# Optimization experiments

Measured on AMD Instinct MI355X. Metric: run time of the kernel, lower is better.

## Reference

```python
import jax, jax.numpy as jnp
import numpy as np

SR = 32000
N_FFT = 1024
HOP = 320
N_MELS = 128
PCEN_S = 0.025
PCEN_ALPHA = 0.98
PCEN_DELTA = 2.0
PCEN_R = 0.5
EPS = 1e-06


def _mel_filterbank():
    # torchaudio melscale_fbanks defaults: HTK mel scale, norm=None, f_min=0, f_max=sr/2
    n_freqs = N_FFT // 2 + 1
    all_freqs = np.linspace(0.0, SR / 2.0, n_freqs)
    def hz_to_mel(f):
        return 2595.0 * np.log10(1.0 + f / 700.0)
    def mel_to_hz(m):
        return 700.0 * (10.0 ** (m / 2595.0) - 1.0)
    m_pts = np.linspace(hz_to_mel(0.0), hz_to_mel(SR / 2.0), N_MELS + 2)
    f_pts = mel_to_hz(m_pts)
    f_diff = f_pts[1:] - f_pts[:-1]                      # (n_mels+1,)
    slopes = f_pts[None, :] - all_freqs[:, None]          # (n_freqs, n_mels+2)
    down = -slopes[:, :-2] / f_diff[:-1]
    up = slopes[:, 2:] / f_diff[1:]
    fb = np.maximum(0.0, np.minimum(down, up))            # (n_freqs, n_mels)
    return jnp.asarray(fb, dtype=jnp.float32)


def _mel_spectrogram(x):
    # x: [B, 1, L]; torch.stft semantics: center=True, reflect pad, periodic hann, power=1
    pad = N_FFT // 2
    xp = jnp.pad(x, ((0, 0), (0, 0), (pad, pad)), mode='reflect')
    L = xp.shape[-1]
    n_frames = 1 + (L - N_FFT) // HOP                      # 401
    idx = jnp.arange(n_frames)[:, None] * HOP + jnp.arange(N_FFT)[None, :]
    frames = xp[..., idx]                                  # [B, 1, T, n_fft]
    n = jnp.arange(N_FFT, dtype=jnp.float32)
    window = 0.5 * (1.0 - jnp.cos(2.0 * jnp.pi * n / N_FFT))  # periodic hann
    spec = jnp.abs(jnp.fft.rfft(frames * window, axis=-1))    # [B, 1, T, F]
    fb = _mel_filterbank()                                    # [F, n_mels]
    mel = jnp.einsum('bctf,fm->bcmt', spec, fb)               # [B, 1, n_mels, T]
    return mel


def _pcen_iir(mel, s):
    # first-order recurrence M_t = (1-s) M_{t-1} + s x_t, M_0 = x_0, along last axis
    xt = jnp.moveaxis(mel, -1, 0)                          # [T, B, 1, M]
    def step(carry, x_t):
        m = (1.0 - s) * carry + s * x_t
        return m, m
    _, rest = jax.lax.scan(step, xt[0], xt[1:])
    M = jnp.concatenate([xt[:1], rest], axis=0)
    return jnp.moveaxis(M, 0, -1)


def setup_inputs() -> dict:
    key = jax.random.key(0)
    x = jax.random.normal(key, (128, 1, 128000), dtype=jnp.float32)
    return {"x": x}


def reference(x):
    mel = _mel_spectrogram(x)                              # [B,1,128,401]
    mel_smooth = _pcen_iir(mel, PCEN_S)
    smooth = jnp.power(EPS + mel_smooth, PCEN_ALPHA)
    pcen = jnp.power(mel / smooth + PCEN_DELTA, PCEN_R) - PCEN_DELTA ** PCEN_R
    mean = jnp.mean(pcen, axis=(2, 3), keepdims=True)
    std = jnp.std(pcen, axis=(2, 3), keepdims=True, ddof=1)  # torch std is unbiased
    return (pcen - mean) / (std + 1e-06)
```

## Files before the change

kernel.cpp:

```cpp
#include <hip/hip_runtime.h>
#include <math.h>

#define SR        32000
#define NFFT      1024
#define HOP       320
#define NMELS     128
#define NFREQS    513
#define LIN       128000
#define PADL      512
#define TFRAMES   401
#define NB        128

#define WS_WIN    0
#define WS_FB     1024
#define WS_FS     66688
#define WS_FE     66816
#define WS_T1     66944
#define WS_T2     68992
#define WS_PART   69120
#define WS_MEL    71168

__global__ void prep_kernel(float* __restrict__ win, float* __restrict__ fb,
                            int* __restrict__ fstart, int* __restrict__ fend,
                            float2* __restrict__ T1, float2* __restrict__ T2) {
    const int tid = threadIdx.x;

    for (int i = tid; i < NFFT; i += 256) {
        double ang = 2.0 * M_PI * (double)i / (double)NFFT;
        win[i] = (float)(0.5 - 0.5 * cos(ang));
    }

    for (int idx = tid; idx < 1024; idx += 256) {
        int tt = idx >> 4, k1 = idx & 15;
        double ang = -2.0 * M_PI * (double)(tt * k1) / 1024.0;
        T1[idx] = make_float2((float)cos(ang), (float)sin(ang));
    }
    if (tid < 64) {
        int s = tid >> 4, k2 = tid & 15;
        double ang = -2.0 * M_PI * (double)(s * k2) / 64.0;
        T2[tid] = make_float2((float)cos(ang), (float)sin(ang));
    }

    if (tid < NMELS) {
        const int m = tid;
        const double mel_max = 2595.0 * log10(1.0 + ((double)SR * 0.5) / 700.0);
        const double m0 = (double)(m)     * mel_max / (double)(NMELS + 1);
        const double m1 = (double)(m + 1) * mel_max / (double)(NMELS + 1);
        const double m2 = (double)(m + 2) * mel_max / (double)(NMELS + 1);
        const double f0 = 700.0 * (pow(10.0, m0 / 2595.0) - 1.0);
        const double f1 = 700.0 * (pow(10.0, m1 / 2595.0) - 1.0);
        const double f2 = 700.0 * (pow(10.0, m2 / 2595.0) - 1.0);
        const double binw = (double)SR * 0.5 / (double)(NFREQS - 1);
        int fs = (int)(f0 / binw) + 1;
        int fe = (int)ceil(f2 / binw);
        fs = (fs > 0) ? fs - 1 : 0;
        fe = (fe < NFREQS) ? fe + 1 : NFREQS;
        for (int f = fs; f < fe; ++f) {
            double freq = (double)f * binw;
            double down = (freq - f0) / (f1 - f0);
            double up   = (f2 - freq) / (f2 - f1);
            double v = fmin(down, up);
            v = fmax(0.0, v);
            fb[f * NMELS + m] = (float)v;
        }
        fstart[m] = fs;
        fend[m]   = fe;
    }
}

__device__ __forceinline__ void dft16(float (&xr)[16], float (&xi)[16]) {
    const float C8 = 0.92387953251128674f;
    const float S8 = 0.38268343236508978f;
    const float R2 = 0.70710678118654752f;
    const float WR[4][4] = {{1,1,1,1},{1, C8, R2, S8},{1, R2, 0.f,-R2},{1, S8,-R2,-C8}};
    const float WI[4][4] = {{0,0,0,0},{0,-S8,-R2,-C8},{0,-R2,-1.f,-R2},{0,-C8,-R2, S8}};
    float pr[4][4], pi[4][4];
#pragma unroll
    for (int j0 = 0; j0 < 4; ++j0) {
        float ar = xr[j0],      ai = xi[j0];
        float br = xr[j0 + 4],  bi = xi[j0 + 4];
        float cr = xr[j0 + 8],  ci = xi[j0 + 8];
        float dr = xr[j0 + 12], di = xi[j0 + 12];
        float t0r = ar + cr, t0i = ai + ci;
        float t1r = ar - cr, t1i = ai - ci;
        float t2r = br + dr, t2i = bi + di;
        float t3r = br - dr, t3i = bi - di;
        pr[j0][0] = t0r + t2r; pi[j0][0] = t0i + t2i;
        pr[j0][1] = t1r + t3i; pi[j0][1] = t1i - t3r;
        pr[j0][2] = t0r - t2r; pi[j0][2] = t0i - t2i;
        pr[j0][3] = t1r - t3i; pi[j0][3] = t1i + t3r;
    }
#pragma unroll
    for (int ka = 0; ka < 4; ++ka) {
        float q0r = pr[0][ka], q0i = pi[0][ka];
        float q1r = pr[1][ka] * WR[1][ka] - pi[1][ka] * WI[1][ka];
        float q1i = pr[1][ka] * WI[1][ka] + pi[1][ka] * WR[1][ka];
        float q2r = pr[2][ka] * WR[2][ka] - pi[2][ka] * WI[2][ka];
        float q2i = pr[2][ka] * WI[2][ka] + pi[2][ka] * WR[2][ka];
        float q3r = pr[3][ka] * WR[3][ka] - pi[3][ka] * WI[3][ka];
        float q3i = pr[3][ka] * WI[3][ka] + pi[3][ka] * WR[3][ka];
        float t0r = q0r + q2r, t0i = q0i + q2i;
        float t1r = q0r - q2r, t1i = q0i - q2i;
        float t2r = q1r + q3r, t2i = q1i + q3i;
        float t3r = q1r - q3r, t3i = q1i - q3i;
        xr[ka]      = t0r + t2r; xi[ka]      = t0i + t2i;
        xr[ka + 4]  = t1r + t3i; xi[ka + 4]  = t1i - t3r;
        xr[ka + 8]  = t0r - t2r; xi[ka + 8]  = t0i - t2i;
        xr[ka + 12] = t1r - t3i; xi[ka + 12] = t1i + t3r;
    }
}

__launch_bounds__(256)
__global__ void fft_mel_kernel(const float* __restrict__ x,
                               const float* __restrict__ win,
                               const float2* __restrict__ T1,
                               const float2* __restrict__ T2,
                               const float* __restrict__ fb,
                               const int* __restrict__ fstart,
                               const int* __restrict__ fend,
                               float* __restrict__ mel) {
    __shared__ __align__(16) float2 buf[4][NFFT];

    const int w = threadIdx.x >> 6;
    const int t = threadIdx.x & 63;
    const int bid  = (blockIdx.x & 7) * 802 + (blockIdx.x >> 3);
    const int task = bid * 4 + w;
    const int q  = task / TFRAMES;
    const int tf = task - q * TFRAMES;
    const float* xb0 = x + (size_t)(2 * q) * LIN;
    const float* xb1 = xb0 + LIN;
    const int base = tf * HOP - PADL;

    float4 t1v[8];
    {
        const float4* T1v = (const float4*)T1;
#pragma unroll
        for (int r = 0; r < 8; ++r) t1v[r] = T1v[t * 8 + r];
    }

    float xr[16], xi[16];
    if (base >= 0 && base + NFFT <= LIN) {
#pragma unroll
        for (int j = 0; j < 16; ++j) {
            int n = t + 64 * j;
            float wv = win[n];
            xr[j] = xb0[base + n] * wv;
            xi[j] = xb1[base + n] * wv;
        }
    } else {
#pragma unroll
        for (int j = 0; j < 16; ++j) {
            int n = t + 64 * j;
            int p = base + n;
            p = (p < 0) ? -p : p;
            p = (p >= LIN) ? (2 * LIN - 2 - p) : p;
            float wv = win[n];
            xr[j] = xb0[p] * wv;
            xi[j] = xb1[p] * wv;
        }
    }

    dft16(xr, xi);
#pragma unroll
    for (int k1 = 1; k1 < 16; ++k1) {
        const int r = k1 >> 1;
        const float2 wv = (k1 & 1) ? make_float2(t1v[r].z, t1v[r].w)
                                   : make_float2(t1v[r].x, t1v[r].y);
        const float tr = xr[k1] * wv.x - xi[k1] * wv.y;
        xi[k1] = xr[k1] * wv.y + xi[k1] * wv.x;
        xr[k1] = tr;
    }

    float2* B = buf[w];
#pragma unroll
    for (int k1 = 0; k1 < 16; ++k1)
        B[k1 * 64 + (t ^ ((k1 & 3) << 2))] = make_float2(xr[k1], xi[k1]);

    const int g = t >> 2, s = t & 3;
    const int c2 = g & 3;
#pragma unroll
    for (int j = 0; j < 16; ++j) {
        float2 v = B[g * 64 + s + 4 * (j ^ c2)];
        xr[j] = v.x; xi[j] = v.y;
    }

    dft16(xr, xi);
    {
        const float2* __restrict__ Tr = T2 + (s << 4);
#pragma unroll
        for (int k2 = 1; k2 < 16; ++k2) {
            const float2 wv = Tr[k2];
            const float tr = xr[k2] * wv.x - xi[k2] * wv.y;
            xi[k2] = xr[k2] * wv.y + xi[k2] * wv.x;
            xr[k2] = tr;
        }
    }

    {
        const int g2 = (g & 7) << 1;
#pragma unroll
        for (int k2 = 0; k2 < 16; ++k2)
            B[g * 64 + ((4 * k2 + s) ^ g2)] = make_float2(xr[k2], xi[k2]);
    }

    const float4* Bv = (const float4*)buf[w];
    const int gk = t & 15;
    const int g2k = (gk & 7) << 1;
    const int tb = t >> 4;
    float m0r[8], m1r[8];
#pragma unroll
    for (int jj = 0; jj < 8; ++jj) {
        const int k  = t + 64 * jj;
        const int jk = (tb + 4 * jj) & 15;
        const int e0 = gk * 64 + ((4 * jk) ^ g2k);
        float4 E01 = Bv[e0 >> 1];
        float4 E23 = Bv[(e0 ^ 2) >> 1];
        float S02r = E01.x + E23.x, S02i = E01.y + E23.y;
        float D02r = E01.x - E23.x, D02i = E01.y - E23.y;
        float S13r = E01.z + E23.z, S13i = E01.w + E23.w;
        float D13r = E01.z - E23.z, D13i = E01.w - E23.w;
        float a, b;
        if (jj < 4) { a = S02r + S13r; b = S02i + S13i; }
        else        { a = D02r + D13i; b = D02i - D13r; }
        const int kN = (1024 - k) & 1023;
        const int gN = kN & 15, jN = (kN >> 4) & 15, bN = kN >> 8;
        const int eN = gN * 64 + ((4 * jN) ^ ((gN & 7) << 1));
        float4 F01 = Bv[eN >> 1];
        float4 F23 = Bv[(eN ^ 2) >> 1];
        float GS02r = F01.x + F23.x, GS02i = F01.y + F23.y;
        float GD02r = F01.x - F23.x, GD02i = F01.y - F23.y;
        float GS13r = F01.z + F23.z, GS13i = F01.w + F23.w;
        float GD13r = F01.z - F23.z, GD13i = F01.w - F23.w;
        const float sE = (bN & 2) ? -1.0f : 1.0f;
        float cEv = GS02r + sE * GS13r, dEv = GS02i + sE * GS13i;
        float cOv = GD02r + sE * GD13i, dOv = GD02i - sE * GD13r;
        float c = (bN & 1) ? cOv : cEv;
        float d = (bN & 1) ? dOv : dEv;
        m0r[jj] = 0.5f * sqrtf((a + c) * (a + c) + (b - d) * (b - d));
        m1r[jj] = 0.5f * sqrtf((b + d) * (b + d) + (c - a) * (c - a));
    }
    float e512a = 0.0f, e512b = 0.0f;
    if (t == 0) {
        float4 E01 = Bv[0], E23 = Bv[1];
        e512a = fabsf((E01.x + E23.x) - (E01.z + E23.z));
        e512b = fabsf((E01.y + E23.y) - (E01.w + E23.w));
    }

    float2* mag2 = buf[w];
#pragma unroll
    for (int jj = 0; jj < 8; ++jj)
        mag2[t + 64 * jj] = make_float2(m0r[jj], m1r[jj]);
    if (t == 0) mag2[512] = make_float2(e512a, e512b);

#pragma unroll
    for (int h = 0; h < 2; ++h) {
        const int m = t + 64 * h;
        const int fs = fstart[m], fe = fend[m];
        const float* fr = fb + m;
        float a0 = 0.0f, a1 = 0.0f;
        for (int f = fs; f < fe; ++f) {
            float2 mg = mag2[f];
            float cf = fr[f * NMELS];
            a0 = fmaf(mg.x, cf, a0);
            a1 = fmaf(mg.y, cf, a1);
        }
        mel[((size_t)(2 * q)     * TFRAMES + tf) * NMELS + m] = a0;
        mel[((size_t)(2 * q + 1) * TFRAMES + tf) * NMELS + m] = a1;
    }
}

#define CHUNKS 8
#define CH0LEN 51
#define CHLEN  50
#define AFACT  0.2819890f

__launch_bounds__(256)
__global__ void pcen_kernel(const float* __restrict__ mel,
                            float* __restrict__ out,
                            double* __restrict__ partials) {
    const int b   = blockIdx.x >> 2;
    const int mg  = blockIdx.x & 3;
    const int tid = threadIdx.x;
    const int ml  = tid & 31;
    const int c   = tid >> 5;
    const int m   = mg * 32 + ml;
    const int t0  = (c == 0) ? 0 : (CH0LEN + CHLEN * (c - 1));
    const int len = (c == 0) ? CH0LEN : CHLEN;
    const float* mb = mel + (size_t)b * TFRAMES * NMELS;

    float v[CH0LEN];
#pragma unroll
    for (int i = 0; i < CH0LEN; ++i)
        if (i < len) v[i] = mb[(size_t)(t0 + i) * NMELS + m];

    float M;
    if (c == 0) {
        M = v[0];
#pragma unroll
        for (int i = 1; i < CH0LEN; ++i) M = fmaf(0.975f, M, 0.025f * v[i]);
    } else {
        M = 0.0f;
#pragma unroll
        for (int i = 0; i < CHLEN; ++i) M = fmaf(0.975f, M, 0.025f * v[i]);
    }
    __shared__ float Bc[CHUNKS][32];
    Bc[c][ml] = M;
    __syncthreads();

    float Min = 0.0f;
    if (c > 0) {
        Min = Bc[0][ml];
        for (int k = 1; k < c; ++k) Min = fmaf(AFACT, Min, Bc[k][ml]);
    }

    M = Min;
    float sum = 0.0f, sumsq = 0.0f;
    float* orow = out + (size_t)b * NMELS * TFRAMES + (size_t)m * TFRAMES + t0;
#pragma unroll
    for (int i = 0; i < CH0LEN; ++i) {
        if (i < len) {
            float xt = v[i];
            M = (c == 0 && i == 0) ? xt : fmaf(0.975f, M, 0.025f * xt);
            float rsm = __expf(-0.98f * __logf(1e-6f + M));
            float p = sqrtf(fmaf(xt, rsm, 2.0f)) - 1.4142135623730951f;
            orow[i] = p;
            sum += p;
            sumsq = fmaf(p, p, sumsq);
        }
    }

    double s = (double)sum, qq = (double)sumsq;
    for (int off = 32; off > 0; off >>= 1) {
        s  += __shfl_down(s, off);
        qq += __shfl_down(qq, off);
    }
    __shared__ double wsum[4], wsq[4];
    const int wid = tid >> 6, lane = tid & 63;
    if (lane == 0) { wsum[wid] = s; wsq[wid] = qq; }
    __syncthreads();
    if (tid == 0) {
        double S = wsum[0] + wsum[1] + wsum[2] + wsum[3];
        double Q = wsq[0] + wsq[1] + wsq[2] + wsq[3];
        partials[(size_t)(b * 4 + mg) * 2]     = S;
        partials[(size_t)(b * 4 + mg) * 2 + 1] = Q;
    }
}

__global__ void norm_kernel(float* __restrict__ out, const double* __restrict__ partials) {
    __shared__ float sh[2];
    const int b = blockIdx.x;
    if (threadIdx.x == 0) {
        double S = 0.0, Q = 0.0;
#pragma unroll
        for (int gg = 0; gg < 4; ++gg) {
            S += partials[(size_t)(b * 4 + gg) * 2];
            Q += partials[(size_t)(b * 4 + gg) * 2 + 1];
        }
        const double n = (double)(NMELS * TFRAMES);
        double mean = S / n;
        double var  = (Q - n * mean * mean) / (n - 1.0);
        double sd   = sqrt(var > 0.0 ? var : 0.0);
        sh[0] = (float)mean;
        sh[1] = (float)(1.0 / (sd + 1e-6));
    }
    __syncthreads();
    const int i4 = blockIdx.y * 256 + threadIdx.x;
    if (i4 >= NMELS * TFRAMES / 4) return;
    const float mean = sh[0], inv = sh[1];
    float4* o = (float4*)(out + (size_t)b * NMELS * TFRAMES);
    float4 vv = o[i4];
    vv.x = (vv.x - mean) * inv;
    vv.y = (vv.y - mean) * inv;
    vv.z = (vv.z - mean) * inv;
    vv.w = (vv.w - mean) * inv;
    o[i4] = vv;
}

extern "C" void kernel_launch(void* const* d_in, const int* in_sizes, int n_in,
                              void* d_out, int out_size, void* d_ws, size_t ws_size,
                              hipStream_t stream) {
    const float* x = (const float*)d_in[0];
    float* out = (float*)d_out;
    float* ws  = (float*)d_ws;

    float*  win    = ws + WS_WIN;
    float*  fb     = ws + WS_FB;
    int*    fstart = (int*)(ws + WS_FS);
    int*    fend   = (int*)(ws + WS_FE);
    float2* T1     = (float2*)(ws + WS_T1);
    float2* T2     = (float2*)(ws + WS_T2);
    double* parts  = (double*)(ws + WS_PART);
    float*  mel    = ws + WS_MEL;

    prep_kernel<<<dim3(1), dim3(256), 0, stream>>>(win, fb, fstart, fend, T1, T2);
    fft_mel_kernel<<<dim3((NB / 2) * TFRAMES / 4), dim3(256), 0, stream>>>(
        x, win, T1, T2, fb, fstart, fend, mel);
    pcen_kernel<<<dim3(NB * 4), dim3(256), 0, stream>>>(mel, out, parts);
    norm_kernel<<<dim3(NB, 51), dim3(256), 0, stream>>>(out, parts);
}
```

Baseline: 234.6 us.

## Pack mel filterbank into fixed-width band table and use one-wave FFT blocks

Replaces the dense 513x128 filterbank and variable-length per-mel loops with a packed 32-wide transposed band table, so the mel projection becomes a fully unrolled fixed loop with coalesced coefficient loads. The FFT/mel kernel moves from 256-thread blocks holding four frames to 64-thread single-wave blocks, and the prep kernel is spread across 9 blocks. The fixed width relies on every mel triangle spanning at most 32 bins, and the shorter bands now do redundant multiply-by-zero work.

```diff
diff --git a/kernel.cpp b/kernel.cpp
--- a/kernel.cpp
+++ b/kernel.cpp
@@ -10,37 +10,40 @@
 #define PADL      512
 #define TFRAMES   401
 #define NB        128
+#define FBW       32
 
 #define WS_WIN    0
-#define WS_FB     1024
-#define WS_FS     66688
-#define WS_FE     66816
-#define WS_T1     66944
-#define WS_T2     68992
-#define WS_PART   69120
-#define WS_MEL    71168
-
-__global__ void prep_kernel(float* __restrict__ win, float* __restrict__ fb,
-                            int* __restrict__ fstart, int* __restrict__ fend,
+#define WS_FBP    1024
+#define WS_FS     5120
+#define WS_T1     5248
+#define WS_T2     7296
+#define WS_PART   7424
+#define WS_MEL    9472
+
+__global__ void prep_kernel(float* __restrict__ win, float* __restrict__ fbpackT,
+                            int* __restrict__ fstart,
                             float2* __restrict__ T1, float2* __restrict__ T2) {
+    const int b   = blockIdx.x;
     const int tid = threadIdx.x;
 
-    for (int i = tid; i < NFFT; i += 256) {
+    if (b < 4) {
+        const int i = b * 256 + tid;
         double ang = 2.0 * M_PI * (double)i / (double)NFFT;
         win[i] = (float)(0.5 - 0.5 * cos(ang));
-    }
-
-    for (int idx = tid; idx < 1024; idx += 256) {
+        return;
+    }
+    if (b < 8) {
+        const int idx = (b - 4) * 256 + tid;
         int tt = idx >> 4, k1 = idx & 15;
         double ang = -2.0 * M_PI * (double)(tt * k1) / 1024.0;
         T1[idx] = make_float2((float)cos(ang), (float)sin(ang));
+        return;
     }
     if (tid < 64) {
         int s = tid >> 4, k2 = tid & 15;
         double ang = -2.0 * M_PI * (double)(s * k2) / 64.0;
         T2[tid] = make_float2((float)cos(ang), (float)sin(ang));
     }
-
     if (tid < NMELS) {
         const int m = tid;
         const double mel_max = 2595.0 * log10(1.0 + ((double)SR * 0.5) / 700.0);
@@ -51,20 +54,23 @@
         const double f1 = 700.0 * (pow(10.0, m1 / 2595.0) - 1.0);
         const double f2 = 700.0 * (pow(10.0, m2 / 2595.0) - 1.0);
         const double binw = (double)SR * 0.5 / (double)(NFREQS - 1);
-        int fs = (int)(f0 / binw) + 1;
-        int fe = (int)ceil(f2 / binw);
-        fs = (fs > 0) ? fs - 1 : 0;
-        fe = (fe < NFREQS) ? fe + 1 : NFREQS;
-        for (int f = fs; f < fe; ++f) {
-            double freq = (double)f * binw;
-            double down = (freq - f0) / (f1 - f0);
-            double up   = (f2 - freq) / (f2 - f1);
-            double v = fmin(down, up);
-            v = fmax(0.0, v);
-            fb[f * NMELS + m] = (float)v;
+        int fs = (int)(f0 / binw);
+        if (fs < 0) fs = 0;
+        int fe = (int)ceil(f2 / binw) + 1;
+        if (fe > NFREQS) fe = NFREQS;
+        for (int i = 0; i < FBW; ++i) {
+            const int f = fs + i;
+            float w = 0.0f;
+            if (f < fe) {
+                double freq = (double)f * binw;
+                double down = (freq - f0) / (f1 - f0);
+                double up   = (f2 - freq) / (f2 - f1);
+                double v = fmin(down, up);
+                w = (float)fmax(0.0, v);
+            }
+            fbpackT[i * NMELS + m] = w;
         }
         fstart[m] = fs;
-        fend[m]   = fe;
     }
 }
 
@@ -110,21 +116,18 @@
     }
 }
 
-__launch_bounds__(256)
+__launch_bounds__(64)
 __global__ void fft_mel_kernel(const float* __restrict__ x,
                                const float* __restrict__ win,
                                const float2* __restrict__ T1,
                                const float2* __restrict__ T2,
-                               const float* __restrict__ fb,
+                               const float* __restrict__ fbpackT,
                                const int* __restrict__ fstart,
-                               const int* __restrict__ fend,
                                float* __restrict__ mel) {
-    __shared__ __align__(16) float2 buf[4][NFFT];
-
-    const int w = threadIdx.x >> 6;
-    const int t = threadIdx.x & 63;
-    const int bid  = (blockIdx.x & 7) * 802 + (blockIdx.x >> 3);
-    const int task = bid * 4 + w;
+    __shared__ __align__(16) float2 buf[NFFT];
+
+    const int t = threadIdx.x;
+    const int task = (blockIdx.x & 7) * 3208 + (blockIdx.x >> 3);
     const int q  = task / TFRAMES;
     const int tf = task - q * TFRAMES;
     const float* xb0 = x + (size_t)(2 * q) * LIN;
@@ -171,7 +174,7 @@
         xr[k1] = tr;
     }
 
-    float2* B = buf[w];
+    float2* B = buf;
 #pragma unroll
     for (int k1 = 0; k1 < 16; ++k1)
         B[k1 * 64 + (t ^ ((k1 & 3) << 2))] = make_float2(xr[k1], xi[k1]);
@@ -203,7 +206,7 @@
             B[g * 64 + ((4 * k2 + s) ^ g2)] = make_float2(xr[k2], xi[k2]);
     }
 
-    const float4* Bv = (const float4*)buf[w];
+    const float4* Bv = (const float4*)buf;
     const int gk = t & 15;
     const int g2k = (gk & 7) << 1;
     const int tb = t >> 4;
@@ -246,7 +249,7 @@
         e512b = fabsf((E01.y + E23.y) - (E01.w + E23.w));
     }
 
-    float2* mag2 = buf[w];
+    float2* mag2 = buf;
 #pragma unroll
     for (int jj = 0; jj < 8; ++jj)
         mag2[t + 64 * jj] = make_float2(m0r[jj], m1r[jj]);
@@ -255,12 +258,14 @@
 #pragma unroll
     for (int h = 0; h < 2; ++h) {
         const int m = t + 64 * h;
-        const int fs = fstart[m], fe = fend[m];
-        const float* fr = fb + m;
+        const int fs = fstart[m];
         float a0 = 0.0f, a1 = 0.0f;
-        for (int f = fs; f < fe; ++f) {
-            float2 mg = mag2[f];
-            float cf = fr[f * NMELS];
+#pragma unroll
+        for (int i = 0; i < FBW; ++i) {
+            const float cf = fbpackT[i * NMELS + m];
+            int f = fs + i;
+            f = (f > 512) ? 512 : f;
+            const float2 mg = mag2[f];
             a0 = fmaf(mg.x, cf, a0);
             a1 = fmaf(mg.y, cf, a1);
         }
@@ -383,18 +388,17 @@
     float* out = (float*)d_out;
     float* ws  = (float*)d_ws;
 
-    float*  win    = ws + WS_WIN;
-    float*  fb     = ws + WS_FB;
-    int*    fstart = (int*)(ws + WS_FS);
-    int*    fend   = (int*)(ws + WS_FE);
-    float2* T1     = (float2*)(ws + WS_T1);
-    float2* T2     = (float2*)(ws + WS_T2);
-    double* parts  = (double*)(ws + WS_PART);
-    float*  mel    = ws + WS_MEL;
-
-    prep_kernel<<<dim3(1), dim3(256), 0, stream>>>(win, fb, fstart, fend, T1, T2);
-    fft_mel_kernel<<<dim3((NB / 2) * TFRAMES / 4), dim3(256), 0, stream>>>(
-        x, win, T1, T2, fb, fstart, fend, mel);
+    float*  win     = ws + WS_WIN;
+    float*  fbpackT = ws + WS_FBP;
+    int*    fstart  = (int*)(ws + WS_FS);
+    float2* T1      = (float2*)(ws + WS_T1);
+    float2* T2      = (float2*)(ws + WS_T2);
+    double* parts   = (double*)(ws + WS_PART);
+    float*  mel     = ws + WS_MEL;
+
+    prep_kernel<<<dim3(9), dim3(256), 0, stream>>>(win, fbpackT, fstart, T1, T2);
+    fft_mel_kernel<<<dim3((NB / 2) * TFRAMES), dim3(64), 0, stream>>>(
+        x, win, T1, T2, fbpackT, fstart, mel);
     pcen_kernel<<<dim3(NB * 4), dim3(256), 0, stream>>>(mel, out, parts);
     norm_kernel<<<dim3(NB, 51), dim3(256), 0, stream>>>(out, parts);
 }
```

Result: faster. 190.3 us (-18.9%).
